# Performance work log

Hardware: AMD Instinct MI355X
Metric: run time of the kernel (lower is better)

## Reference

```python
import jax, jax.numpy as jnp
import numpy as np

NUM_GRAPHS = 64
NODES_PER_GRAPH = 256
EDGES_PER_GRAPH = 1024
D_FEAT = 512
H_FIL = 1024
H_PHI = 256
N_CLASSES = 10


def _xavier(k, fan_in, fan_out):
    s = float(np.sqrt(6.0 / (fan_in + fan_out)))
    return jax.random.uniform(k, (fan_in, fan_out), jnp.float32, -s, s)


def setup_inputs() -> dict:
    key = jax.random.key(0)
    ks = jax.random.split(key, 8)
    N = NUM_GRAPHS * NODES_PER_GRAPH
    x = jax.random.normal(ks[0], (N, D_FEAT), jnp.float32)
    # per-graph local edge endpoints, offset to global vertex ids
    el = jax.random.randint(ks[1], (NUM_GRAPHS, EDGES_PER_GRAPH, 2), 0, NODES_PER_GRAPH)
    offs = (jnp.arange(NUM_GRAPHS) * NODES_PER_GRAPH)[:, None, None]
    edges = (el + offs).reshape(-1, 2).astype(jnp.int32)
    sample_id = jnp.repeat(jnp.arange(NUM_GRAPHS, dtype=jnp.int32), NODES_PER_GRAPH)
    return {
        "x": x,
        "edges": edges,
        "sample_id": sample_id,
        "w_fil1": _xavier(ks[2], D_FEAT, H_FIL),
        "b_fil1": jnp.full((H_FIL,), 0.01, jnp.float32),
        "w_fil2": _xavier(ks[3], H_FIL, 1),
        "b_fil2": jnp.full((1,), 0.01, jnp.float32),
        "w_phi0": _xavier(ks[4], 2, H_PHI),
        "b_phi0": jnp.full((H_PHI,), 0.01, jnp.float32),
        "w_phi1": _xavier(ks[5], 2, H_PHI),
        "b_phi1": jnp.full((H_PHI,), 0.01, jnp.float32),
        "w_head": _xavier(ks[6], 2 * H_PHI, N_CLASSES),
        "b_head": jnp.full((N_CLASSES,), 0.01, jnp.float32),
    }


def vertex_persistence_deaths(f, edges):
    """0-dim sublevel-set persistence of a vertex filtration via union-find.

    Returns death value per vertex (birth is f[v]):
      - vertices killed by an edge merge (elder rule) die at max(f_u, f_v);
      - per-component survivors (essential classes) are paired with the
        max filtration value of their component (extended persistence).
    Pairing indices are discrete; death VALUES stay differentiable w.r.t. f.
    """
    N = f.shape[0]
    w = jnp.maximum(f[edges[:, 0]], f[edges[:, 1]])
    order = jnp.argsort(w)  # process edges in increasing filtration order
    eu, ev, ew = edges[order, 0], edges[order, 1], w[order]

    def find(parent, u):
        return jax.lax.while_loop(lambda r: parent[r] != r, lambda r: parent[r], u)

    def body(carry, uvw):
        parent, death, paired = carry
        u, v, wv = uvw
        ru = find(parent, u)
        rv = find(parent, v)
        # path compression of the two endpoints
        parent = parent.at[u].set(ru).at[v].set(rv)
        u_elder = (f[ru] < f[rv]) | ((f[ru] == f[rv]) & (ru < rv))
        elder = jnp.where(u_elder, ru, rv)
        young = jnp.where(u_elder, rv, ru)
        merge = ru != rv
        parent = parent.at[young].set(jnp.where(merge, elder, parent[young]))
        death = death.at[young].set(jnp.where(merge, wv, death[young]))
        paired = paired.at[young].set(paired[young] | merge)
        return (parent, death, paired), None

    init = (jnp.arange(N, dtype=eu.dtype), jnp.zeros(N, f.dtype), jnp.zeros(N, bool))
    (parent, death, paired), _ = jax.lax.scan(body, init, (eu, ev, ew))
    # full path compression by repeated pointer jumping (integer-only)
    parent = jax.lax.while_loop(lambda p: jnp.any(p[p] != p), lambda p: p[p], parent)
    comp_max = jnp.full((N,), -jnp.inf, f.dtype).at[parent].max(f)
    return jnp.where(paired, death, comp_max[parent])


def reference(x, edges, sample_id, w_fil1, b_fil1, w_fil2, b_fil2,
              w_phi0, b_phi0, w_phi1, b_phi1, w_head, b_head):
    # fil: node filtration in (0, 1)
    h = jax.nn.relu(x @ w_fil1 + b_fil1)
    f = jax.nn.sigmoid(h @ w_fil2 + b_fil2)[:, 0]  # [N]

    # sublevel persistence -> h0 pairs (birth, death), one per vertex
    d_sub = vertex_persistence_deaths(f, edges)
    h0 = jnp.stack([f, d_sub], axis=1)  # [N, 2]

    # superlevel persistence via -f, then negate & swap -> h1 pairs
    d_sup = vertex_persistence_deaths(-f, edges)
    h1 = jnp.stack([-d_sup, f], axis=1)  # (-death_sup, -birth_sup) = (-d_sup, f)

    # cls: per-pair MLP + sum pooling per graph, linear head
    phi0 = jax.nn.relu(h0 @ w_phi0 + b_phi0)  # [N, H_PHI]
    phi1 = jax.nn.relu(h1 @ w_phi1 + b_phi1)
    p0 = jax.ops.segment_sum(phi0, sample_id, num_segments=NUM_GRAPHS)
    p1 = jax.ops.segment_sum(phi1, sample_id, num_segments=NUM_GRAPHS)
    feats = jnp.concatenate([p0, p1], axis=1)  # [B, 2*H_PHI]
    return feats @ w_head + b_head  # [B, N_CLASSES]
```

## Files before the change

kernel.cpp:

```cpp
#include <hip/hip_runtime.h>
#include <hip/hip_bf16.h>

#define NUM_GRAPHS 64
#define NODES 256
#define EDGES 1024
#define NTOT (NUM_GRAPHS * NODES)
#define DF 512
#define HF 1024
#define HP 256
#define NC 10
#define INF32 0xFFFFFFFFu

typedef short bf16x8 __attribute__((ext_vector_type(8)));
typedef float f32x4 __attribute__((ext_vector_type(4)));

__device__ __forceinline__ unsigned short bf16r(float f) {
    __hip_bfloat16 h = __float2bfloat16(f);
    return *(unsigned short*)&h;
}
__device__ __forceinline__ unsigned encf(float x) {
    union { float f; unsigned u; } c; c.f = x;
    return (c.u & 0x80000000u) ? ~c.u : (c.u | 0x80000000u);
}

__global__ __launch_bounds__(256) void k_cvt_frag(
    const float* __restrict__ w1, unsigned short* __restrict__ w1f)
{
    __shared__ float ls[128 * 16];
    const int tid = threadIdx.x;
    const int cg = blockIdx.x >> 2, kq = blockIdx.x & 3;
    const int c = tid & 15, kr = tid >> 4;
#pragma unroll
    for (int it = 0; it < 8; ++it) {
        int kk = it * 16 + kr;
        ls[kk * 16 + c] = w1[(size_t)(kq * 128 + kk) * HF + cg * 16 + c];
    }
    __syncthreads();
    const int tt = tid >> 6, n16 = tid & 15, q = (tid >> 4) & 3;
    unsigned short v[8];
#pragma unroll
    for (int j = 0; j < 8; ++j)
        v[j] = bf16r(ls[(tt * 32 + q * 8 + j) * 16 + n16]);
    size_t off = ((size_t)(cg * 16 + kq * 4 + tt) * 64 + (q * 16 + n16)) * 8;
#pragma unroll
    for (int j = 0; j < 8; ++j) w1f[off + j] = v[j];
}

__global__ __launch_bounds__(256, 1) void k_fil_mfma(
    const float* __restrict__ x, const unsigned short* __restrict__ w1f,
    const float* __restrict__ b1, const float* __restrict__ w2,
    float* __restrict__ zbuf)
{
    __shared__ unsigned short Bbuf[4 * 16 * 512];
    __shared__ float zpart[4][32];
    const int tid = threadIdx.x;
    const int lane = tid & 63;
    const int wv = tid >> 6;
    const int l15 = lane & 15, quad = lane >> 4;
    const int half = wv >> 1;
    const int rt = wv & 1;
    const int r0 = blockIdx.x * 64;
    const int rowA = r0 + rt * 32 + l15;
    const int rowB = rowA + 16;

    bf16x8 A0[16], A1[16];
#pragma unroll
    for (int t = 0; t < 16; ++t) {
        const float* s0 = x + (size_t)rowA * DF + t * 32 + quad * 8;
        const float* s1 = x + (size_t)rowB * DF + t * 32 + quad * 8;
        float4 a = *(const float4*)s0, b = *(const float4*)(s0 + 4);
        float4 c = *(const float4*)s1, d = *(const float4*)(s1 + 4);
        A0[t][0]=(short)bf16r(a.x); A0[t][1]=(short)bf16r(a.y);
        A0[t][2]=(short)bf16r(a.z); A0[t][3]=(short)bf16r(a.w);
        A0[t][4]=(short)bf16r(b.x); A0[t][5]=(short)bf16r(b.y);
        A0[t][6]=(short)bf16r(b.z); A0[t][7]=(short)bf16r(b.w);
        A1[t][0]=(short)bf16r(c.x); A1[t][1]=(short)bf16r(c.y);
        A1[t][2]=(short)bf16r(c.z); A1[t][3]=(short)bf16r(c.w);
        A1[t][4]=(short)bf16r(d.x); A1[t][5]=(short)bf16r(d.y);
        A1[t][6]=(short)bf16r(d.z); A1[t][7]=(short)bf16r(d.w);
    }

    const int t128 = tid & 127;
    const int sh = tid >> 7;
    uint4 pf[8];
    {
        const uint4* s = (const uint4*)(w1f + (size_t)(sh * 32) * 8192);
#pragma unroll
        for (int j = 0; j < 8; ++j) pf[j] = s[t128 + j * 128];
        uint4* d = (uint4*)Bbuf + (sh * 2 + 0) * 1024;
#pragma unroll
        for (int j = 0; j < 8; ++j) d[t128 + j * 128] = pf[j];
    }
    __syncthreads();

    float s_[2][4] = {{0,0,0,0},{0,0,0,0}};

    for (int i = 0; i < 32; ++i) {
        const int par = i & 1;
        if (i < 31) {
            const uint4* s = (const uint4*)(w1f + (size_t)(sh * 32 + i + 1) * 8192);
#pragma unroll
            for (int j = 0; j < 8; ++j) pf[j] = s[t128 + j * 128];
        }
        const unsigned short* bb = Bbuf + (half * 2 + par) * 8192 + lane * 8;
        f32x4 a00={0,0,0,0}, a01={0,0,0,0}, a10={0,0,0,0}, a11={0,0,0,0};
#pragma unroll
        for (int t = 0; t < 8; ++t) {
            bf16x8 Bf0 = *(const bf16x8*)(bb + t * 512);
            bf16x8 Bf1 = *(const bf16x8*)(bb + (t + 8) * 512);
            a00 = __builtin_amdgcn_mfma_f32_16x16x32_bf16(A0[t], Bf0, a00, 0, 0, 0);
            a10 = __builtin_amdgcn_mfma_f32_16x16x32_bf16(A1[t], Bf0, a10, 0, 0, 0);
            a01 = __builtin_amdgcn_mfma_f32_16x16x32_bf16(A0[t + 8], Bf1, a01, 0, 0, 0);
            a11 = __builtin_amdgcn_mfma_f32_16x16x32_bf16(A1[t + 8], Bf1, a11, 0, 0, 0);
        }
        const int col = (half * 32 + i) * 16 + l15;
        const float b1c = b1[col], w2c = w2[col];
#pragma unroll
        for (int r = 0; r < 4; ++r) {
            float h0 = (a00[r] + a01[r]) + b1c; h0 = h0 > 0.f ? h0 : 0.f;
            s_[0][r] = fmaf(h0, w2c, s_[0][r]);
            float h1 = (a10[r] + a11[r]) + b1c; h1 = h1 > 0.f ? h1 : 0.f;
            s_[1][r] = fmaf(h1, w2c, s_[1][r]);
        }
        if (i < 31) {
            uint4* d = (uint4*)Bbuf + (sh * 2 + (par ^ 1)) * 1024;
#pragma unroll
            for (int j = 0; j < 8; ++j) d[t128 + j * 128] = pf[j];
        }
        __syncthreads();
    }

#pragma unroll
    for (int sub = 0; sub < 2; ++sub)
#pragma unroll
        for (int r = 0; r < 4; ++r) {
            float v = s_[sub][r];
            v += __shfl_xor(v, 1, 16);
            v += __shfl_xor(v, 2, 16);
            v += __shfl_xor(v, 4, 16);
            v += __shfl_xor(v, 8, 16);
            if (l15 == 0) zpart[wv][sub * 16 + quad * 4 + r] = v;
        }
    __syncthreads();
    if (tid < 64) {
        int rrt = tid >> 5, idx = tid & 31;
        zbuf[r0 + tid] = zpart[rrt][idx] + zpart[rrt + 2][idx];
    }
}

#define TN2 16
__global__ __launch_bounds__(256) void k_fil(
    const float* __restrict__ x, const float* __restrict__ w1,
    const float* __restrict__ b1, const float* __restrict__ w2,
    float* __restrict__ zout)
{
    __shared__ float xs[TN2][DF];
    __shared__ float part[256];
    const int tid = threadIdx.x;
    const int n0 = blockIdx.x * TN2;
    for (int c = tid; c < TN2 * DF / 4; c += 256) {
        int n = c >> 7, k4 = (c & 127) << 2;
        *(float4*)&xs[n][k4] = *(const float4*)(x + (size_t)(n0 + n) * DF + k4);
    }
    __syncthreads();
    float h[TN2][4];
#pragma unroll
    for (int n = 0; n < TN2; ++n)
#pragma unroll
        for (int q = 0; q < 4; ++q) h[n][q] = 0.f;
    for (int k = 0; k < DF; ++k) {
        float wr[4];
#pragma unroll
        for (int q = 0; q < 4; ++q) wr[q] = w1[(size_t)k * HF + tid + 256 * q];
#pragma unroll
        for (int n = 0; n < TN2; ++n) {
            float xv = xs[n][k];
#pragma unroll
            for (int q = 0; q < 4; ++q) h[n][q] = fmaf(xv, wr[q], h[n][q]);
        }
    }
    float b1r[4], w2r[4];
#pragma unroll
    for (int q = 0; q < 4; ++q) { b1r[q] = b1[tid + 256 * q]; w2r[q] = w2[tid + 256 * q]; }
    for (int n = 0; n < TN2; ++n) {
        float s = 0.f;
#pragma unroll
        for (int q = 0; q < 4; ++q) {
            float hv = h[n][q] + b1r[q];
            s += (hv > 0.f ? hv : 0.f) * w2r[q];
        }
        part[tid] = s;
        __syncthreads();
        for (int off = 128; off > 0; off >>= 1) {
            if (tid < off) part[tid] += part[tid + off];
            __syncthreads();
        }
        if (tid == 0) zout[n0 + n] = part[0];
        __syncthreads();
    }
}

__global__ __launch_bounds__(512) void k_pers(
    const int* __restrict__ edges, const float* __restrict__ zbuf,
    const float* __restrict__ b2, float* __restrict__ dout )
{
    const int bid = blockIdx.x;
    const int g = bid >> 1, sgn = bid & 1;
    const int tid = threadIdx.x;
    const int v = tid & 255, vh = tid >> 8;

    __shared__ float fv[NODES];
    __shared__ unsigned long long vkey[NODES];
    __shared__ int order_[NODES], rank_[NODES];
    __shared__ float fvr[NODES];
    __shared__ unsigned eks[EDGES];
    __shared__ int comp[NODES];
    __shared__ unsigned minE[NODES];
    __shared__ int nxt[NODES], par2[NODES];
    __shared__ unsigned char mstflag[EDGES];
    __shared__ int cnt, chg;
    __shared__ unsigned mstK[NODES], srt[NODES];
    __shared__ int par[NODES], dr[NODES], cmaxr[NODES];
    __shared__ int rkp[512];

    if (tid < 256) {
        float z0 = zbuf[g * NODES + tid];
        float f0 = 1.f / (1.f + expf(-(z0 + b2[0])));
        fv[tid] = sgn ? -f0 : f0;
        vkey[tid] = ((unsigned long long)encf(fv[tid]) << 32) | (unsigned)tid;
        srt[tid] = INF32; dr[tid] = -1; cmaxr[tid] = 0; par[tid] = tid;
        comp[tid] = tid;
    }
    __syncthreads();

    {
        const unsigned long long mk = vkey[v];
        const int j0 = vh << 7;
        int c = 0;
#pragma unroll 8
        for (int j = j0; j < j0 + 128; ++j) c += (vkey[j] < mk) ? 1 : 0;
        rkp[tid] = c;
    }
    __syncthreads();
    if (tid < 256) {
        int rk = rkp[tid] + rkp[tid + 256];
        order_[rk] = tid;
        rank_[tid] = rk;
        fvr[rk] = fv[tid];
    }
    __syncthreads();

#pragma unroll
    for (int q = 0; q < 2; ++q) {
        int e = tid + q * 512;
        int u = edges[2 * (g * EDGES + e)]     - g * NODES;
        int w = edges[2 * (g * EDGES + e) + 1] - g * NODES;
        if (u == w) { eks[e] = INF32; }
        else {
            int ra = rank_[u], rb = rank_[w];
            int rlo = ra < rb ? ra : rb, rhi = ra < rb ? rb : ra;
            eks[e] = ((unsigned)rhi << 18) | ((unsigned)e << 8) | (unsigned)rlo;
        }
        mstflag[e] = 0;
    }
    __syncthreads();

    for (int round = 0; round < 8; ++round) {
        if (tid < 256) minE[tid] = INF32;
        if (tid == 0) chg = 0;
        __syncthreads();
#pragma unroll
        for (int q = 0; q < 2; ++q) {
            int e = tid + q * 512;
            unsigned k = eks[e];
            if (k != INF32) {
                int rlo = (int)(k & 255u), rhi = (int)(k >> 18);
                int cu = comp[rlo], cv = comp[rhi];
                if (cu != cv) {
                    atomicMin(&minE[cu], k);
                    atomicMin(&minE[cv], k);
                } else if (!mstflag[e]) {
                    eks[e] = INF32;
                }
            }
        }
        __syncthreads();
        if (tid < 256) {
            unsigned mk = minE[tid];
            int o = tid;
            if (mk != INF32) {
                int rlo = (int)(mk & 255u), rhi = (int)(mk >> 18);
                int cu = comp[rlo], cv = comp[rhi];
                o = (cu == tid) ? cv : cu;
                mstflag[(mk >> 8) & 0x3FFu] = 1;
                chg = 1;
            }
            nxt[tid] = o;
        }
        __syncthreads();
        if (!chg) break;
        if (tid < 256) {
            int o = nxt[tid];
            int p = o;
            if (nxt[o] == tid && tid < o) p = tid;
            par2[tid] = p;
        }
        __syncthreads();
        for (;;) {
            int p = par2[par2[v]];
            int done = __syncthreads_and(p == par2[v]);
            if (done) break;
            par2[v] = p;
            __syncthreads();
        }
        if (tid < 256) comp[tid] = par2[comp[tid]];
        __syncthreads();
    }

    if (tid == 0) cnt = 0;
    __syncthreads();
#pragma unroll
    for (int q = 0; q < 2; ++q) {
        int e = tid + q * 512;
        if (mstflag[e]) {
            int p = atomicAdd(&cnt, 1);
            mstK[p] = eks[e];
        }
    }
    __syncthreads();
    if (tid < 256 && tid >= cnt) mstK[tid] = INF32;
    __syncthreads();

    {
        const unsigned m2 = mstK[v];
        const int j0 = vh << 7;
        int c = 0;
        if (m2 != INF32) {
#pragma unroll 8
            for (int j = j0; j < j0 + 128; ++j) c += (mstK[j] < m2) ? 1 : 0;
        }
        rkp[tid] = c;
    }
    __syncthreads();
    if (tid < 256) {
        unsigned m2 = mstK[tid];
        if (m2 != INF32) srt[rkp[tid] + rkp[tid + 256]] = m2;
    }
    __syncthreads();

    if (tid < 64) {
        const int ln = tid;
        int r0 = ln, r1 = 64 + ln, r2 = 128 + ln, r3 = 192 + ln;
        int d0 = -1, d1 = -1, d2 = -1, d3 = -1;
        int sv0 = (int)srt[ln], sv1 = (int)srt[ln + 64];
        int sv2 = (int)srt[ln + 128], sv3 = (int)srt[ln + 192];
        const int n = cnt;
        for (int blk = 0; blk < 4; ++blk) {
            const int base = blk << 6;
            if (base >= n) break;
            int lim = n - base; if (lim > 64) lim = 64;
            const int svb = blk == 0 ? sv0 : blk == 1 ? sv1 : blk == 2 ? sv2 : sv3;
            for (int sl = 0; sl < lim; ++sl) {
                unsigned k = (unsigned)__builtin_amdgcn_readlane(svb, sl);
                const int rlo = (int)(k & 255u);
                const int rhi = (int)(k >> 18);
                const int jl = rlo >> 6, jh = rhi >> 6;
                const int cl = jl == 0 ? r0 : jl == 1 ? r1 : jl == 2 ? r2 : r3;
                const int a = __builtin_amdgcn_readlane(cl, rlo & 63);
                const int ch = jh == 0 ? r0 : jh == 1 ? r1 : jh == 2 ? r2 : r3;
                const int b = __builtin_amdgcn_readlane(ch, rhi & 63);
                if (a != b) {
                    const int elder = a < b ? a : b, young = a < b ? b : a;
                    r0 = (r0 == young) ? elder : r0;
                    r1 = (r1 == young) ? elder : r1;
                    r2 = (r2 == young) ? elder : r2;
                    r3 = (r3 == young) ? elder : r3;
                    const int jy = young >> 6;
                    const bool own = (ln == (young & 63));
                    if (jy == 0)      { if (own) d0 = rhi; }
                    else if (jy == 1) { if (own) d1 = rhi; }
                    else if (jy == 2) { if (own) d2 = rhi; }
                    else              { if (own) d3 = rhi; }
                }
            }
        }
        par[ln] = r0; par[ln + 64] = r1; par[ln + 128] = r2; par[ln + 192] = r3;
        dr[ln] = d0; dr[ln + 64] = d1; dr[ln + 128] = d2; dr[ln + 192] = d3;
    }
    __syncthreads();

    if (tid < 256) {
        const int r = par[tid];
        atomicMax(&cmaxr[r], tid);
    }
    __syncthreads();

    if (tid < 256) {
        const int r = par[tid];
        float dv = (dr[tid] >= 0) ? fvr[dr[tid]] : fvr[cmaxr[r]];
        dout[sgn * NTOT + g * NODES + order_[tid]] = dv;
    }
}

__global__ __launch_bounds__(256) void k_head(
    const float* __restrict__ zbuf, const float* __restrict__ b2,
    const float* __restrict__ dbuf,
    const float* __restrict__ wp0, const float* __restrict__ bp0,
    const float* __restrict__ wp1, const float* __restrict__ bp1,
    const float* __restrict__ wh, const float* __restrict__ bh,
    float* __restrict__ out)
{
    const int g = blockIdx.x, tid = threadIdx.x;
    const int lane = tid & 63, wv = tid >> 6;
    __shared__ float lf[NODES], l0[NODES], l1[NODES];
    __shared__ float wpart[4][NC];
    lf[tid] = 1.f / (1.f + expf(-(zbuf[g * NODES + tid] + b2[0])));
    l0[tid] = dbuf[g * NODES + tid];
    l1[tid] = dbuf[NTOT + g * NODES + tid];
    __syncthreads();
    const float w00 = wp0[tid], w01 = wp0[HP + tid], bb0 = bp0[tid];
    const float w10 = wp1[tid], w11 = wp1[HP + tid], bb1 = bp1[tid];
    float s0 = 0.f, s1 = 0.f;
    for (int n = 0; n < NODES; ++n) {
        float f = lf[n], d0 = l0[n], d1 = l1[n];
        float a0 = fmaf(f, w00, fmaf(d0, w01, bb0));
        float a1 = fmaf(-d1, w10, fmaf(f, w11, bb1));
        s0 += a0 > 0.f ? a0 : 0.f;
        s1 += a1 > 0.f ? a1 : 0.f;
    }
    float pc[NC];
    const float* whr0 = wh + (size_t)tid * NC;
    const float* whr1 = wh + (size_t)(HP + tid) * NC;
#pragma unroll
    for (int c = 0; c < NC; ++c) pc[c] = s0 * whr0[c] + s1 * whr1[c];
#pragma unroll
    for (int off = 32; off > 0; off >>= 1)
#pragma unroll
        for (int c = 0; c < NC; ++c) pc[c] += __shfl_xor(pc[c], off, 64);
    if (lane == 0)
#pragma unroll
        for (int c = 0; c < NC; ++c) wpart[wv][c] = pc[c];
    __syncthreads();
    if (tid < NC)
        out[g * NC + tid] = bh[tid] + wpart[0][tid] + wpart[1][tid]
                          + wpart[2][tid] + wpart[3][tid];
}

extern "C" void kernel_launch(void* const* d_in, const int* in_sizes, int n_in,
                              void* d_out, int out_size, void* d_ws, size_t ws_size,
                              hipStream_t stream)
{
    const float* x   = (const float*)d_in[0];
    const int*   edg = (const int*)d_in[1];
    const float* w1  = (const float*)d_in[3];
    const float* b1  = (const float*)d_in[4];
    const float* w2  = (const float*)d_in[5];
    const float* b2  = (const float*)d_in[6];
    const float* wp0 = (const float*)d_in[7];
    const float* bp0 = (const float*)d_in[8];
    const float* wp1 = (const float*)d_in[9];
    const float* bp1 = (const float*)d_in[10];
    const float* wh  = (const float*)d_in[11];
    const float* bh  = (const float*)d_in[12];

    float* zbuf = (float*)d_ws;
    float* dbuf = zbuf + NTOT;
    unsigned short* w1f = (unsigned short*)(dbuf + 2 * NTOT);

    const size_t WS_REQ = (size_t)3 * NTOT * 4 + (size_t)HF * DF * 2 + 256;

    if (ws_size >= WS_REQ) {
        k_cvt_frag<<<256, 256, 0, stream>>>(w1, w1f);
        k_fil_mfma<<<256, 256, 0, stream>>>(x, w1f, b1, w2, zbuf);
    } else {
        k_fil     <<<NTOT / TN2, 256, 0, stream>>>(x, w1, b1, w2, zbuf);
    }
    k_pers<<<NUM_GRAPHS * 2, 512, 0, stream>>>(edg, zbuf, b2, dbuf);
    k_head<<<NUM_GRAPHS, 256, 0, stream>>>(zbuf, b2, dbuf, wp0, bp0, wp1, bp1,
                                           wh, bh, (float*)d_out);
}
```

Before: 209.8 us.

## Fuse persistence and head kernels, one block per graph covering both filtrations

Merges the persistence kernel and the classification-head kernel into a single kernel launched with one 512-thread block per graph. Each half of the block runs the sublevel or superlevel union-find on its own shared-memory arrays. Death values stay in shared memory and feed the per-pair MLP and sum pooling directly. This removes one launch and the global write and read of the death buffer. In exchange, each thread's rank loops now scan all 256 keys instead of half, and both filtrations share one block-wide barrier schedule and convergence flag.

```diff
diff --git a/kernel.cpp b/kernel.cpp
--- a/kernel.cpp
+++ b/kernel.cpp
@@ -200,161 +200,155 @@
     }
 }
 
-__global__ __launch_bounds__(512) void k_pers(
+__global__ __launch_bounds__(512) void k_pers_head(
     const int* __restrict__ edges, const float* __restrict__ zbuf,
-    const float* __restrict__ b2, float* __restrict__ dout )
+    const float* __restrict__ b2,
+    const float* __restrict__ wp0, const float* __restrict__ bp0,
+    const float* __restrict__ wp1, const float* __restrict__ bp1,
+    const float* __restrict__ wh, const float* __restrict__ bh,
+    float* __restrict__ out)
 {
-    const int bid = blockIdx.x;
-    const int g = bid >> 1, sgn = bid & 1;
+    const int g = blockIdx.x;
     const int tid = threadIdx.x;
-    const int v = tid & 255, vh = tid >> 8;
-
-    __shared__ float fv[NODES];
-    __shared__ unsigned long long vkey[NODES];
-    __shared__ int order_[NODES], rank_[NODES];
-    __shared__ float fvr[NODES];
-    __shared__ unsigned eks[EDGES];
-    __shared__ int comp[NODES];
-    __shared__ unsigned minE[NODES];
-    __shared__ int nxt[NODES], par2[NODES];
-    __shared__ unsigned char mstflag[EDGES];
-    __shared__ int cnt, chg;
-    __shared__ unsigned mstK[NODES], srt[NODES];
-    __shared__ int par[NODES], dr[NODES], cmaxr[NODES];
-    __shared__ int rkp[512];
-
-    if (tid < 256) {
-        float z0 = zbuf[g * NODES + tid];
-        float f0 = 1.f / (1.f + expf(-(z0 + b2[0])));
-        fv[tid] = sgn ? -f0 : f0;
-        vkey[tid] = ((unsigned long long)encf(fv[tid]) << 32) | (unsigned)tid;
-        srt[tid] = INF32; dr[tid] = -1; cmaxr[tid] = 0; par[tid] = tid;
-        comp[tid] = tid;
-    }
-    __syncthreads();
-
-    {
-        const unsigned long long mk = vkey[v];
-        const int j0 = vh << 7;
-        int c = 0;
+    const int hs = tid >> 8;
+    const int t = tid & 255;
+
+    __shared__ float fv[2][NODES];
+    __shared__ unsigned long long vkey[2][NODES];
+    __shared__ int order_[2][NODES], rank_[2][NODES];
+    __shared__ float fvr[2][NODES];
+    __shared__ unsigned eks[2][EDGES];
+    __shared__ int comp[2][NODES];
+    __shared__ unsigned minE[2][NODES];
+    __shared__ int nxt[2][NODES], par2[2][NODES];
+    __shared__ unsigned char mstflag[2][EDGES];
+    __shared__ int cnt[2];
+    __shared__ int chg;
+    __shared__ unsigned mstK[2][NODES], srt[2][NODES];
+    __shared__ int par[2][NODES], dr[2][NODES], cmaxr[2][NODES];
+    __shared__ float dsv[2][NODES];
+    __shared__ float sred0[512], sred1[512];
+    __shared__ float wpart[4][NC];
+
+    float z0 = zbuf[g * NODES + t];
+    float f0 = 1.f / (1.f + expf(-(z0 + b2[0])));
+    float fvt = hs ? -f0 : f0;
+    fv[hs][t] = fvt;
+    unsigned long long myk = ((unsigned long long)encf(fvt) << 32) | (unsigned)t;
+    vkey[hs][t] = myk;
+    srt[hs][t] = INF32; dr[hs][t] = -1; cmaxr[hs][t] = 0; par[hs][t] = t;
+    comp[hs][t] = t;
+    __syncthreads();
+
+    {
+        int rk = 0;
 #pragma unroll 8
-        for (int j = j0; j < j0 + 128; ++j) c += (vkey[j] < mk) ? 1 : 0;
-        rkp[tid] = c;
-    }
-    __syncthreads();
-    if (tid < 256) {
-        int rk = rkp[tid] + rkp[tid + 256];
-        order_[rk] = tid;
-        rank_[tid] = rk;
-        fvr[rk] = fv[tid];
-    }
-    __syncthreads();
-
-#pragma unroll
-    for (int q = 0; q < 2; ++q) {
-        int e = tid + q * 512;
+        for (int j = 0; j < NODES; ++j) rk += (vkey[hs][j] < myk) ? 1 : 0;
+        order_[hs][rk] = t;
+        rank_[hs][t] = rk;
+        fvr[hs][rk] = fvt;
+    }
+    __syncthreads();
+
+#pragma unroll
+    for (int q = 0; q < 4; ++q) {
+        int e = t + q * 256;
         int u = edges[2 * (g * EDGES + e)]     - g * NODES;
         int w = edges[2 * (g * EDGES + e) + 1] - g * NODES;
-        if (u == w) { eks[e] = INF32; }
+        if (u == w) { eks[hs][e] = INF32; }
         else {
-            int ra = rank_[u], rb = rank_[w];
+            int ra = rank_[hs][u], rb = rank_[hs][w];
             int rlo = ra < rb ? ra : rb, rhi = ra < rb ? rb : ra;
-            eks[e] = ((unsigned)rhi << 18) | ((unsigned)e << 8) | (unsigned)rlo;
-        }
-        mstflag[e] = 0;
+            eks[hs][e] = ((unsigned)rhi << 18) | ((unsigned)e << 8) | (unsigned)rlo;
+        }
+        mstflag[hs][e] = 0;
     }
     __syncthreads();
 
     for (int round = 0; round < 8; ++round) {
-        if (tid < 256) minE[tid] = INF32;
+        minE[hs][t] = INF32;
         if (tid == 0) chg = 0;
         __syncthreads();
 #pragma unroll
-        for (int q = 0; q < 2; ++q) {
-            int e = tid + q * 512;
-            unsigned k = eks[e];
+        for (int q = 0; q < 4; ++q) {
+            int e = t + q * 256;
+            unsigned k = eks[hs][e];
             if (k != INF32) {
                 int rlo = (int)(k & 255u), rhi = (int)(k >> 18);
-                int cu = comp[rlo], cv = comp[rhi];
+                int cu = comp[hs][rlo], cv = comp[hs][rhi];
                 if (cu != cv) {
-                    atomicMin(&minE[cu], k);
-                    atomicMin(&minE[cv], k);
-                } else if (!mstflag[e]) {
-                    eks[e] = INF32;
+                    atomicMin(&minE[hs][cu], k);
+                    atomicMin(&minE[hs][cv], k);
+                } else if (!mstflag[hs][e]) {
+                    eks[hs][e] = INF32;
                 }
             }
         }
         __syncthreads();
-        if (tid < 256) {
-            unsigned mk = minE[tid];
-            int o = tid;
+        {
+            unsigned mk = minE[hs][t];
+            int o = t;
             if (mk != INF32) {
                 int rlo = (int)(mk & 255u), rhi = (int)(mk >> 18);
-                int cu = comp[rlo], cv = comp[rhi];
-                o = (cu == tid) ? cv : cu;
-                mstflag[(mk >> 8) & 0x3FFu] = 1;
+                int cu = comp[hs][rlo], cv = comp[hs][rhi];
+                o = (cu == t) ? cv : cu;
+                mstflag[hs][(mk >> 8) & 0x3FFu] = 1;
                 chg = 1;
             }
-            nxt[tid] = o;
+            nxt[hs][t] = o;
         }
         __syncthreads();
         if (!chg) break;
-        if (tid < 256) {
-            int o = nxt[tid];
+        {
+            int o = nxt[hs][t];
             int p = o;
-            if (nxt[o] == tid && tid < o) p = tid;
-            par2[tid] = p;
+            if (nxt[hs][o] == t && t < o) p = t;
+            par2[hs][t] = p;
         }
         __syncthreads();
         for (;;) {
-            int p = par2[par2[v]];
-            int done = __syncthreads_and(p == par2[v]);
+            int p = par2[hs][par2[hs][t]];
+            int done = __syncthreads_and(p == par2[hs][t]);
             if (done) break;
-            par2[v] = p;
+            par2[hs][t] = p;
             __syncthreads();
         }
-        if (tid < 256) comp[tid] = par2[comp[tid]];
-        __syncthreads();
-    }
-
-    if (tid == 0) cnt = 0;
-    __syncthreads();
-#pragma unroll
-    for (int q = 0; q < 2; ++q) {
-        int e = tid + q * 512;
-        if (mstflag[e]) {
-            int p = atomicAdd(&cnt, 1);
-            mstK[p] = eks[e];
-        }
-    }
-    __syncthreads();
-    if (tid < 256 && tid >= cnt) mstK[tid] = INF32;
-    __syncthreads();
-
-    {
-        const unsigned m2 = mstK[v];
-        const int j0 = vh << 7;
-        int c = 0;
-        if (m2 != INF32) {
+        comp[hs][t] = par2[hs][comp[hs][t]];
+        __syncthreads();
+    }
+
+    if (t == 0) cnt[hs] = 0;
+    __syncthreads();
+#pragma unroll
+    for (int q = 0; q < 4; ++q) {
+        int e = t + q * 256;
+        if (mstflag[hs][e]) {
+            int p = atomicAdd(&cnt[hs], 1);
+            mstK[hs][p] = eks[hs][e];
+        }
+    }
+    __syncthreads();
+    if (t >= cnt[hs]) mstK[hs][t] = INF32;
+    __syncthreads();
+
+    {
+        unsigned myk2 = mstK[hs][t];
+        if (myk2 != INF32) {
+            int pos = 0;
 #pragma unroll 8
-            for (int j = j0; j < j0 + 128; ++j) c += (mstK[j] < m2) ? 1 : 0;
-        }
-        rkp[tid] = c;
-    }
-    __syncthreads();
-    if (tid < 256) {
-        unsigned m2 = mstK[tid];
-        if (m2 != INF32) srt[rkp[tid] + rkp[tid + 256]] = m2;
-    }
-    __syncthreads();
-
-    if (tid < 64) {
-        const int ln = tid;
+            for (int j = 0; j < NODES; ++j) pos += (mstK[hs][j] < myk2) ? 1 : 0;
+            srt[hs][pos] = myk2;
+        }
+    }
+    __syncthreads();
+
+    if (t < 64) {
+        const int ln = t;
         int r0 = ln, r1 = 64 + ln, r2 = 128 + ln, r3 = 192 + ln;
         int d0 = -1, d1 = -1, d2 = -1, d3 = -1;
-        int sv0 = (int)srt[ln], sv1 = (int)srt[ln + 64];
-        int sv2 = (int)srt[ln + 128], sv3 = (int)srt[ln + 192];
-        const int n = cnt;
+        int sv0 = (int)srt[hs][ln], sv1 = (int)srt[hs][ln + 64];
+        int sv2 = (int)srt[hs][ln + 128], sv3 = (int)srt[hs][ln + 192];
+        const int n = cnt[hs];
         for (int blk = 0; blk < 4; ++blk) {
             const int base = blk << 6;
             if (base >= n) break;
@@ -384,62 +378,57 @@
                 }
             }
         }
-        par[ln] = r0; par[ln + 64] = r1; par[ln + 128] = r2; par[ln + 192] = r3;
-        dr[ln] = d0; dr[ln + 64] = d1; dr[ln + 128] = d2; dr[ln + 192] = d3;
-    }
-    __syncthreads();
-
+        par[hs][ln] = r0; par[hs][ln + 64] = r1;
+        par[hs][ln + 128] = r2; par[hs][ln + 192] = r3;
+        dr[hs][ln] = d0; dr[hs][ln + 64] = d1;
+        dr[hs][ln + 128] = d2; dr[hs][ln + 192] = d3;
+    }
+    __syncthreads();
+
+    {
+        const int r = par[hs][t];
+        atomicMax(&cmaxr[hs][r], t);
+    }
+    __syncthreads();
+    {
+        const int r = par[hs][t];
+        float dvv = (dr[hs][t] >= 0) ? fvr[hs][dr[hs][t]] : fvr[hs][cmaxr[hs][r]];
+        dsv[hs][order_[hs][t]] = dvv;
+    }
+    __syncthreads();
+
+    {
+        const float w00 = wp0[t], w01 = wp0[HP + t], bb0 = bp0[t];
+        const float w10 = wp1[t], w11 = wp1[HP + t], bb1 = bp1[t];
+        float s0 = 0.f, s1 = 0.f;
+        const int n0 = hs * 128;
+        for (int n = n0; n < n0 + 128; ++n) {
+            float f = fv[0][n], dd0 = dsv[0][n], dd1 = dsv[1][n];
+            float a0 = fmaf(f, w00, fmaf(dd0, w01, bb0));
+            float a1 = fmaf(-dd1, w10, fmaf(f, w11, bb1));
+            s0 += a0 > 0.f ? a0 : 0.f;
+            s1 += a1 > 0.f ? a1 : 0.f;
+        }
+        sred0[tid] = s0; sred1[tid] = s1;
+    }
+    __syncthreads();
     if (tid < 256) {
-        const int r = par[tid];
-        atomicMax(&cmaxr[r], tid);
-    }
-    __syncthreads();
-
-    if (tid < 256) {
-        const int r = par[tid];
-        float dv = (dr[tid] >= 0) ? fvr[dr[tid]] : fvr[cmaxr[r]];
-        dout[sgn * NTOT + g * NODES + order_[tid]] = dv;
-    }
-}
-
-__global__ __launch_bounds__(256) void k_head(
-    const float* __restrict__ zbuf, const float* __restrict__ b2,
-    const float* __restrict__ dbuf,
-    const float* __restrict__ wp0, const float* __restrict__ bp0,
-    const float* __restrict__ wp1, const float* __restrict__ bp1,
-    const float* __restrict__ wh, const float* __restrict__ bh,
-    float* __restrict__ out)
-{
-    const int g = blockIdx.x, tid = threadIdx.x;
-    const int lane = tid & 63, wv = tid >> 6;
-    __shared__ float lf[NODES], l0[NODES], l1[NODES];
-    __shared__ float wpart[4][NC];
-    lf[tid] = 1.f / (1.f + expf(-(zbuf[g * NODES + tid] + b2[0])));
-    l0[tid] = dbuf[g * NODES + tid];
-    l1[tid] = dbuf[NTOT + g * NODES + tid];
-    __syncthreads();
-    const float w00 = wp0[tid], w01 = wp0[HP + tid], bb0 = bp0[tid];
-    const float w10 = wp1[tid], w11 = wp1[HP + tid], bb1 = bp1[tid];
-    float s0 = 0.f, s1 = 0.f;
-    for (int n = 0; n < NODES; ++n) {
-        float f = lf[n], d0 = l0[n], d1 = l1[n];
-        float a0 = fmaf(f, w00, fmaf(d0, w01, bb0));
-        float a1 = fmaf(-d1, w10, fmaf(f, w11, bb1));
-        s0 += a0 > 0.f ? a0 : 0.f;
-        s1 += a1 > 0.f ? a1 : 0.f;
-    }
-    float pc[NC];
-    const float* whr0 = wh + (size_t)tid * NC;
-    const float* whr1 = wh + (size_t)(HP + tid) * NC;
-#pragma unroll
-    for (int c = 0; c < NC; ++c) pc[c] = s0 * whr0[c] + s1 * whr1[c];
-#pragma unroll
-    for (int off = 32; off > 0; off >>= 1)
-#pragma unroll
-        for (int c = 0; c < NC; ++c) pc[c] += __shfl_xor(pc[c], off, 64);
-    if (lane == 0)
-#pragma unroll
-        for (int c = 0; c < NC; ++c) wpart[wv][c] = pc[c];
+        const int lane = tid & 63, wv = tid >> 6;
+        float s0 = sred0[tid] + sred0[tid + 256];
+        float s1 = sred1[tid] + sred1[tid + 256];
+        float pc[NC];
+        const float* whr0 = wh + (size_t)tid * NC;
+        const float* whr1 = wh + (size_t)(HP + tid) * NC;
+#pragma unroll
+        for (int c = 0; c < NC; ++c) pc[c] = s0 * whr0[c] + s1 * whr1[c];
+#pragma unroll
+        for (int off = 32; off > 0; off >>= 1)
+#pragma unroll
+            for (int c = 0; c < NC; ++c) pc[c] += __shfl_xor(pc[c], off, 64);
+        if (lane == 0)
+#pragma unroll
+            for (int c = 0; c < NC; ++c) wpart[wv][c] = pc[c];
+    }
     __syncthreads();
     if (tid < NC)
         out[g * NC + tid] = bh[tid] + wpart[0][tid] + wpart[1][tid]
@@ -475,7 +464,7 @@
     } else {
         k_fil     <<<NTOT / TN2, 256, 0, stream>>>(x, w1, b1, w2, zbuf);
     }
-    k_pers<<<NUM_GRAPHS * 2, 512, 0, stream>>>(edg, zbuf, b2, dbuf);
-    k_head<<<NUM_GRAPHS, 256, 0, stream>>>(zbuf, b2, dbuf, wp0, bp0, wp1, bp1,
-                                           wh, bh, (float*)d_out);
-}
+    k_pers_head<<<NUM_GRAPHS, 512, 0, stream>>>(edg, zbuf, b2, wp0, bp0,
+                                                wp1, bp1, wh, bh,
+                                                (float*)d_out);
+}
```

New measurement: 221.4 us. 1.06x slower.

## Pack union-find roots into bytes with SWAR updates and exit Boruvka early

Applied to the files above, without the earlier changes.

The single-wave elder-rule union-find now keeps the four 8-bit root labels per lane in one packed 32-bit register. Relabelling uses SWAR byte-equality masks instead of four compares and selects, and death ranks are packed into bytes the same way, with 0 serving as the unpaired sentinel. Because the bit trick replaces the branch, every MST edge pays the same fixed instruction count. The Boruvka loop also gains an extra block-wide check that exits once all vertices share one component. The 0 sentinel relies on rank 0 never being a death rank, which holds because a death is always the higher endpoint.

```diff
diff --git a/kernel.cpp b/kernel.cpp
--- a/kernel.cpp
+++ b/kernel.cpp
@@ -228,7 +228,7 @@
         float f0 = 1.f / (1.f + expf(-(z0 + b2[0])));
         fv[tid] = sgn ? -f0 : f0;
         vkey[tid] = ((unsigned long long)encf(fv[tid]) << 32) | (unsigned)tid;
-        srt[tid] = INF32; dr[tid] = -1; cmaxr[tid] = 0; par[tid] = tid;
+        srt[tid] = INF32; dr[tid] = 0; cmaxr[tid] = 0; par[tid] = tid;
         comp[tid] = tid;
     }
     __syncthreads();
@@ -315,6 +315,7 @@
         }
         if (tid < 256) comp[tid] = par2[comp[tid]];
         __syncthreads();
+        if (__syncthreads_and(comp[v] == comp[0])) break;
     }
 
     if (tid == 0) cnt = 0;
@@ -350,8 +351,8 @@
 
     if (tid < 64) {
         const int ln = tid;
-        int r0 = ln, r1 = 64 + ln, r2 = 128 + ln, r3 = 192 + ln;
-        int d0 = -1, d1 = -1, d2 = -1, d3 = -1;
+        unsigned rpack = (unsigned)ln * 0x01010101u + 0xC0804000u;
+        unsigned dpack = 0u;
         int sv0 = (int)srt[ln], sv1 = (int)srt[ln + 64];
         int sv2 = (int)srt[ln + 128], sv3 = (int)srt[ln + 192];
         const int n = cnt;
@@ -361,31 +362,36 @@
             int lim = n - base; if (lim > 64) lim = 64;
             const int svb = blk == 0 ? sv0 : blk == 1 ? sv1 : blk == 2 ? sv2 : sv3;
             for (int sl = 0; sl < lim; ++sl) {
-                unsigned k = (unsigned)__builtin_amdgcn_readlane(svb, sl);
-                const int rlo = (int)(k & 255u);
-                const int rhi = (int)(k >> 18);
-                const int jl = rlo >> 6, jh = rhi >> 6;
-                const int cl = jl == 0 ? r0 : jl == 1 ? r1 : jl == 2 ? r2 : r3;
-                const int a = __builtin_amdgcn_readlane(cl, rlo & 63);
-                const int ch = jh == 0 ? r0 : jh == 1 ? r1 : jh == 2 ? r2 : r3;
-                const int b = __builtin_amdgcn_readlane(ch, rhi & 63);
-                if (a != b) {
-                    const int elder = a < b ? a : b, young = a < b ? b : a;
-                    r0 = (r0 == young) ? elder : r0;
-                    r1 = (r1 == young) ? elder : r1;
-                    r2 = (r2 == young) ? elder : r2;
-                    r3 = (r3 == young) ? elder : r3;
-                    const int jy = young >> 6;
-                    const bool own = (ln == (young & 63));
-                    if (jy == 0)      { if (own) d0 = rhi; }
-                    else if (jy == 1) { if (own) d1 = rhi; }
-                    else if (jy == 2) { if (own) d2 = rhi; }
-                    else              { if (own) d3 = rhi; }
-                }
+                const unsigned k = (unsigned)__builtin_amdgcn_readlane(svb, sl);
+                const int lo = (int)(k & 255u);
+                const int hi = (int)((k >> 18) & 255u);
+                const unsigned va = (unsigned)__builtin_amdgcn_readlane((int)rpack, lo & 63);
+                const int ca = (int)((va >> ((lo >> 6) << 3)) & 255u);
+                const unsigned vb = (unsigned)__builtin_amdgcn_readlane((int)rpack, hi & 63);
+                const int cb = (int)((vb >> ((hi >> 6) << 3)) & 255u);
+                const int elder = ca < cb ? ca : cb;
+                const int young = ca > cb ? ca : cb;
+                const unsigned y4 = (unsigned)young * 0x01010101u;
+                const unsigned d4 = (unsigned)(young ^ elder) * 0x01010101u;
+                const unsigned mm = rpack ^ y4;
+                const unsigned ww = (mm | 0x80808080u) - 0x01010101u;
+                const unsigned zm = ~(ww | mm) & 0x80808080u;
+                rpack ^= d4 & ((zm >> 7) * 255u);
+                const int merged = (ca != cb) ? 1 : 0;
+                const int ysel = merged ? (young & 63) : 64;
+                const unsigned shy = (unsigned)((young >> 6) << 3);
+                const unsigned nd = (dpack & ~(255u << shy)) | ((unsigned)hi << shy);
+                dpack = (ln == ysel) ? nd : dpack;
             }
         }
-        par[ln] = r0; par[ln + 64] = r1; par[ln + 128] = r2; par[ln + 192] = r3;
-        dr[ln] = d0; dr[ln + 64] = d1; dr[ln + 128] = d2; dr[ln + 192] = d3;
+        par[ln]       = (int)(rpack & 255u);
+        par[ln + 64]  = (int)((rpack >> 8) & 255u);
+        par[ln + 128] = (int)((rpack >> 16) & 255u);
+        par[ln + 192] = (int)(rpack >> 24);
+        dr[ln]        = (int)(dpack & 255u);
+        dr[ln + 64]   = (int)((dpack >> 8) & 255u);
+        dr[ln + 128]  = (int)((dpack >> 16) & 255u);
+        dr[ln + 192]  = (int)(dpack >> 24);
     }
     __syncthreads();
 
@@ -397,7 +403,8 @@
 
     if (tid < 256) {
         const int r = par[tid];
-        float dv = (dr[tid] >= 0) ? fvr[dr[tid]] : fvr[cmaxr[r]];
+        const int db = dr[tid];
+        float dv = (db != 0) ? fvr[db] : fvr[cmaxr[r]];
         dout[sgn * NTOT + g * NODES + order_[tid]] = dv;
     }
 }
```

New measurement: 187.1 us. -10.8%, faster.
